# Kernel tuning notes

Measured on AMD Instinct MI355X. Metric: run time of the kernel, lower is better.

## Reference

```python
import jax, jax.numpy as jnp
import numpy as np

B, GRID, IN_CO, OUT_CO = 32, 4096, 64, 64
T_EMB, N_MODES = 256, 512
M_HALF = N_MODES // 2 + 1  # 257 retained rFFT modes


def setup_inputs() -> dict:
    key = jax.random.key(0)
    ks = jax.random.split(key, 6)
    w_std = jnp.sqrt(1.0 / (2.0 * IN_CO))
    return {
        "x": jax.random.normal(ks[0], (B, GRID, IN_CO), jnp.float32),
        "t_emb": jax.random.normal(ks[1], (B, T_EMB), jnp.float32),
        "weights_real": jax.random.normal(ks[2], (M_HALF, IN_CO, OUT_CO), jnp.float32) * w_std,
        "weights_imag": jax.random.normal(ks[3], (M_HALF, IN_CO, OUT_CO), jnp.float32) * w_std,
        "dense_real": jax.random.normal(ks[4], (T_EMB, M_HALF), jnp.float32) * jnp.sqrt(1.0 / T_EMB),
        "dense_imag": jax.random.normal(ks[5], (T_EMB, M_HALF), jnp.float32) * jnp.sqrt(1.0 / T_EMB),
    }


def reference(x, t_emb, weights_real, weights_imag, dense_real, dense_imag):
    b, in_grid_sz, _ = x.shape
    m = weights_real.shape[0]  # n_modes//2 + 1
    weights = weights_real + 1j * weights_imag  # (m, in_co, out_co)
    # rFFT over the grid axis
    x_ft = jnp.fft.rfft(x, axis=-2, norm="forward")  # (b, grid//2+1, in_co) complex
    # time modulation per mode: Dense(real) + i*Dense(imag)
    t_tr = (t_emb @ dense_real) + 1j * (t_emb @ dense_imag)  # (b, m)
    # original einsum with eye == elementwise per-mode scale then per-mode matmul
    x_out = jnp.einsum("bmi,mio->bmo", x_ft[:, :m, :], weights) * t_tr[:, :, None]
    out_ft = jnp.zeros((b, in_grid_sz // 2 + 1, weights.shape[-1]), jnp.complex64)
    out_ft = out_ft.at[:, :m, :].set(x_out)
    return jnp.fft.irfft(out_ft, axis=-2, n=in_grid_sz, norm="forward")
```

## Files before the change

kernel.cpp:

```cpp
#include <hip/hip_runtime.h>
#include <hip/hip_bf16.h>

typedef short short8 __attribute__((ext_vector_type(8)));
typedef float f32x4 __attribute__((ext_vector_type(4)));
typedef const void __attribute__((address_space(1))) as1_void;
typedef void __attribute__((address_space(3))) as3_void;

__device__ __forceinline__ float sin_rev(float r) {
  float o; asm("v_sin_f32 %0, %1" : "=v"(o) : "v"(r)); return o;
}
__device__ __forceinline__ float cos_rev(float r) {
  float o; asm("v_cos_f32 %0, %1" : "=v"(o) : "v"(r)); return o;
}

#define INV4096 0.000244140625f
#define INV16   0.0625f

__global__ __launch_bounds__(256) void prep_kernel(const float* __restrict__ t_emb,
                                                   const float* __restrict__ dr,
                                                   const float* __restrict__ di,
                                                   float* __restrict__ Sr,
                                                   float* __restrict__ Si,
                                                   const float* __restrict__ x,
                                                   __hip_bfloat16* __restrict__ E,
                                                   __hip_bfloat16* __restrict__ O,
                                                   float* __restrict__ Xr256p,
                                                   float* __restrict__ x2048f) {
  const int bid = blockIdx.x;
  const int tid = threadIdx.x;
  __shared__ float te[256];
  __shared__ float tileA[64][65];
  __shared__ float tileB[64][65];
  __shared__ float red[4][64];
  __shared__ float xm[64];

  if (bid < 32) {
    int b = bid;
    te[tid] = t_emb[b * 256 + tid];
    __syncthreads();
    for (int m = tid; m < 257; m += 256) {
      float ar = 0.f, ai = 0.f;
      for (int t = 0; t < 256; ++t) {
        float e = te[t];
        ar += e * dr[t * 257 + m];
        ai += e * di[t * 257 + m];
      }
      float c = (m == 0 ? 1.0f : 2.0f) * (1.0f / 4096.0f);
      Sr[b * 257 + m] = ar * c;
      Si[b * 257 + m] = ai * c;
    }
  } else {
    int idx = bid - 32;
    int nt = idx & 31;
    int b  = idx >> 5;
    int n0 = nt * 64;
    int m0r = (63 - nt) * 64;
#pragma unroll
    for (int it = 0; it < 4; ++it) {
      int c = it * 256 + tid;
      int r = c >> 4, i4 = (c & 15) * 4;
      float4 v = *(const float4*)&x[((size_t)b * 4096 + n0 + r) * 64 + i4];
      tileA[r][i4 + 0] = v.x; tileA[r][i4 + 1] = v.y;
      tileA[r][i4 + 2] = v.z; tileA[r][i4 + 3] = v.w;
      float4 w = *(const float4*)&x[((size_t)b * 4096 + m0r + r) * 64 + i4];
      tileB[r][i4 + 0] = w.x; tileB[r][i4 + 1] = w.y;
      tileB[r][i4 + 2] = w.z; tileB[r][i4 + 3] = w.w;
    }
    if (tid < 64) xm[tid] = (nt > 0) ? x[((size_t)b * 4096 + (4096 - n0)) * 64 + tid] : 0.f;
    __syncthreads();
#pragma unroll
    for (int it = 0; it < 2; ++it) {
      int c  = it * 256 + tid;
      int i  = c >> 3;
      int ch = c & 7;
      union { short8 v; unsigned short u[8]; } pe, po;
#pragma unroll
      for (int jj = 0; jj < 8; ++jj) {
        int j = ch * 8 + jj;
        float a = tileA[j][i];
        float mir = (j == 0) ? xm[i] : tileB[64 - j][i];
        __hip_bfloat16 he = __float2bfloat16(a + mir);
        __hip_bfloat16 ho = __float2bfloat16(a - mir);
        pe.u[jj] = *(unsigned short*)&he;
        po.u[jj] = *(unsigned short*)&ho;
      }
      size_t base = ((size_t)b * 64 + i) * 2048 + n0 + ch * 8;
      *(short8*)&E[base] = pe.v;
      *(short8*)&O[base] = po.v;
    }
    {
      int i = tid & 63, g = tid >> 6;
      float acc = 0.f;
#pragma unroll
      for (int j = 0; j < 16; ++j) {
        float w = cos_rev((float)j * INV16);
        acc += w * (tileA[g * 16 + j][i] + tileB[g * 16 + j][i]);
      }
      red[g][i] = acc;
    }
    __syncthreads();
    if (tid < 64) {
      Xr256p[((size_t)b * 32 + nt) * 64 + tid] =
          red[0][tid] + red[1][tid] + red[2][tid] + red[3][tid];
      if (nt == 31) x2048f[b * 64 + tid] = tileB[0][tid];
    }
  }
}

template <int NF, int MODE>
__device__ __forceinline__ void stage_genT(int m0, int kt,
                                           const __hip_bfloat16* __restrict__ B, int ldb, int n0,
                                           __hip_bfloat16* As, __hip_bfloat16* Bs, int tid) {
#pragma unroll
  for (int j = 0; j < NF; ++j) {
    int c   = j * 256 + tid;
    int row = c >> 3;
    int chg = (c & 7) ^ (row & 7);
    const __hip_bfloat16* gb = B + (size_t)(n0 + row) * ldb + kt + chg * 8;
    __hip_bfloat16* lb = Bs + (size_t)(j * 256 + (tid & 192)) * 8;
    __builtin_amdgcn_global_load_lds((as1_void*)gb, (as3_void*)lb, 16, 0, 0);
  }
#pragma unroll
  for (int j = 0; j < 4; ++j) {
    int c   = j * 256 + tid;
    int row = c >> 3;
    int chg = (c & 7) ^ (row & 7);
    int gr  = m0 + row;
    union { short8 v; unsigned short u[8]; } pk;
#pragma unroll
    for (int jj = 0; jj < 8; ++jj) {
      int col = kt + chg * 8 + jj;
      float v;
      if (MODE == 1) {
        int m  = (gr < 256) ? gr : (gr - 255);
        int ph = (m * col) & 4095;
        v = (gr < 256) ?  cos_rev((float)ph * INV4096)
                       : -sin_rev((float)ph * INV4096);
      } else {
        int k  = (col < 256) ? col : (col - 255);
        int ph = (gr * k) & 4095;
        v = (col < 256) ? cos_rev((float)ph * INV4096)
                        : sin_rev((float)ph * INV4096);
      }
      __hip_bfloat16 h = __float2bfloat16(v);
      pk.u[jj] = *(unsigned short*)&h;
    }
    *(short8*)&As[(size_t)c * 8] = pk.v;
  }
}

template <int NF>
__device__ __forceinline__ void compute_stepT(const __hip_bfloat16* As, const __hip_bfloat16* Bs,
                                              int wr, int wc, int fr, int fq,
                                              f32x4 acc[4][NF]) {
#pragma unroll
  for (int kk = 0; kk < 2; ++kk) {
    short8 av[4], bv[NF];
#pragma unroll
    for (int m = 0; m < 4; ++m) {
      int row  = wr + m * 16 + fr;
      int slot = (fq + kk * 4) ^ (row & 7);
      av[m] = *(const short8*)(As + row * 64 + slot * 8);
    }
#pragma unroll
    for (int n = 0; n < NF; ++n) {
      int row  = wc + n * 16 + fr;
      int slot = (fq + kk * 4) ^ (row & 7);
      bv[n] = *(const short8*)(Bs + row * 64 + slot * 8);
    }
#pragma unroll
    for (int m = 0; m < 4; ++m)
#pragma unroll
      for (int n = 0; n < NF; ++n)
        acc[m][n] = __builtin_amdgcn_mfma_f32_16x16x32_bf16(av[m], bv[n], acc[m][n], 0, 0, 0);
  }
}

template <int NF, int MODE>
__device__ __forceinline__ void gemm_coreT(int m0,
                                           const __hip_bfloat16* __restrict__ B, int ldb, int n0,
                                           int k0, int ksteps,
                                           __hip_bfloat16* As, __hip_bfloat16* Bs,
                                           f32x4 acc[4][NF]) {
  const int tid  = threadIdx.x;
  const int lane = tid & 63;
  const int wv   = tid >> 6;
  const int wr   = (wv >> 1) * 64;
  const int wc   = (wv & 1) * (NF * 16);
  const int fr   = lane & 15;
  const int fq   = lane >> 4;

  for (int ks = 0; ks < ksteps; ++ks) {
    stage_genT<NF, MODE>(m0, k0 + ks * 64, B, ldb, n0, As, Bs, tid);
    __syncthreads();
    compute_stepT<NF>(As, Bs, wr, wc, fr, fq, acc);
    __syncthreads();
  }
}

__global__ __launch_bounds__(256) void gemm1_kernel(const __hip_bfloat16* __restrict__ E,
                                                    const __hip_bfloat16* __restrict__ O,
                                                    __hip_bfloat16* __restrict__ C1,
                                                    int kchunk, int splitk) {
  __shared__ __hip_bfloat16 As[128 * 64];
  __shared__ __hip_bfloat16 Bs[128 * 64];
  int n0 = blockIdx.x * 128;
  int m0 = blockIdx.y * 128;
  int k0 = blockIdx.z * kchunk;
  const __hip_bfloat16* B = (m0 < 256) ? E : O;
  f32x4 acc[4][4];
#pragma unroll
  for (int m = 0; m < 4; ++m)
#pragma unroll
    for (int n = 0; n < 4; ++n)
#pragma unroll
      for (int r = 0; r < 4; ++r) acc[m][n][r] = 0.f;

  gemm_coreT<4, 1>(m0, B, 2048, n0, k0, kchunk >> 6, As, Bs, acc);

  const int lane = threadIdx.x & 63;
  const int wv   = threadIdx.x >> 6;
  const int wr   = (wv >> 1) * 64, wc = (wv & 1) * 64;
  const int fr   = lane & 15, fq = lane >> 4;
#pragma unroll
  for (int m = 0; m < 4; ++m)
#pragma unroll
    for (int n = 0; n < 4; ++n)
#pragma unroll
      for (int j = 0; j < 4; ++j) {
        int row = m0 + wr + m * 16 + fq * 4 + j;
        int col = n0 + wc + n * 16 + fr;
        C1[((size_t)row * splitk + blockIdx.z) * 2048 + col] = __float2bfloat16(acc[m][n][j]);
      }
}

__global__ __launch_bounds__(256) void mix_kernel(const __hip_bfloat16* __restrict__ C1,
                                                  const float* __restrict__ Xr256p,
                                                  const float* __restrict__ x2048f,
                                                  const float* __restrict__ Wr,
                                                  const float* __restrict__ Wi,
                                                  const float* __restrict__ Sr,
                                                  const float* __restrict__ Si,
                                                  __hip_bfloat16* __restrict__ Y2T,
                                                  __hip_bfloat16* __restrict__ Yx,
                                                  int splitk) {
  const int k = blockIdx.x;
  const int q = blockIdx.y;
  const int tid = threadIdx.x;
  __shared__ float wlr[4096];
  __shared__ float wli[4096];
  __shared__ float xs[2048];

  const float* wrg = Wr + (size_t)k * 4096;
  const float* wig = Wi + (size_t)k * 4096;
  for (int c = tid; c < 1024; c += 256) {
    *(float4*)&wlr[c * 4] = *(const float4*)&wrg[c * 4];
    *(float4*)&wli[c * 4] = *(const float4*)&wig[c * 4];
  }

  {
    const int part = tid >> 7;
    const int ln   = tid & 127;
    const int bi0  = q * 1024 + ln * 8;
    float f[8] = {0.f, 0.f, 0.f, 0.f, 0.f, 0.f, 0.f, 0.f};
    if (part == 0) {
      if (k < 256) {
        const __hip_bfloat16* src = C1 + (size_t)k * splitk * 2048 + bi0;
        for (int z = 0; z < splitk; ++z) {
          short8 v = *(const short8*)(src + (size_t)z * 2048);
#pragma unroll
          for (int j = 0; j < 8; ++j) {
            unsigned short u = (unsigned short)v[j];
            f[j] += __bfloat162float(*(__hip_bfloat16*)&u);
          }
        }
        float par = (k & 1) ? -1.f : 1.f;
#pragma unroll
        for (int j = 0; j < 8; ++j) f[j] += par * x2048f[bi0 + j];
      } else {
        const float* sp = Xr256p + (size_t)(bi0 >> 6) * 2048 + (bi0 & 63);
#pragma unroll 8
        for (int nt = 0; nt < 32; ++nt)
#pragma unroll
          for (int j = 0; j < 8; ++j) f[j] += sp[nt * 64 + j];
      }
    } else if (k > 0) {
      const __hip_bfloat16* src = C1 + (size_t)(255 + k) * splitk * 2048 + bi0;
      for (int z = 0; z < splitk; ++z) {
        short8 v = *(const short8*)(src + (size_t)z * 2048);
#pragma unroll
        for (int j = 0; j < 8; ++j) {
          unsigned short u = (unsigned short)v[j];
          f[j] += __bfloat162float(*(__hip_bfloat16*)&u);
        }
      }
    }
#pragma unroll
    for (int j = 0; j < 8; ++j) xs[part * 1024 + ln * 8 + j] = f[j];
  }
  __syncthreads();

  const int o  = tid & 63;
  const int jj = tid >> 6;
  float pr[4] = {0.f, 0.f, 0.f, 0.f};
  float pi[4] = {0.f, 0.f, 0.f, 0.f};
#pragma unroll 4
  for (int i = 0; i < 64; ++i) {
    float wrv = wlr[i * 64 + o];
    float wiv = wli[i * 64 + o];
#pragma unroll
    for (int u = 0; u < 4; ++u) {
      int lb = (jj * 4 + u) * 64 + i;
      float xr = xs[lb], xi = xs[1024 + lb];
      pr[u] += xr * wrv - xi * wiv;
      pi[u] += xr * wiv + xi * wrv;
    }
  }
#pragma unroll
  for (int u = 0; u < 4; ++u) {
    int b = q * 16 + jj * 4 + u;
    float sr = Sr[b * 257 + k], si = Si[b * 257 + k];
    int bo = b * 64 + o;
    __hip_bfloat16 yr = __float2bfloat16(pr[u] * sr - pi[u] * si);
    __hip_bfloat16 yi = __float2bfloat16(pr[u] * si + pi[u] * sr);
    if (k < 256) Y2T[(size_t)bo * 512 + k] = yr;
    else         Yx[bo] = yr;
    if (k >= 1)  Y2T[(size_t)bo * 512 + 255 + k] = yi;
  }
}

__global__ __launch_bounds__(256) void gemm2_kernel(const __hip_bfloat16* __restrict__ Y2T,
                                                    const __hip_bfloat16* __restrict__ Yx,
                                                    float* __restrict__ out) {
  __shared__ __hip_bfloat16 As[128 * 64];
  __shared__ __hip_bfloat16 Bs[64 * 64];
  __shared__ float red2[4][64];
  int n0 = blockIdx.x * 64;
  int m0 = blockIdx.y * 128;
  f32x4 accC[4][2], accS[4][2];
#pragma unroll
  for (int m = 0; m < 4; ++m)
#pragma unroll
    for (int n = 0; n < 2; ++n)
#pragma unroll
      for (int r = 0; r < 4; ++r) { accC[m][n][r] = 0.f; accS[m][n][r] = 0.f; }

  gemm_coreT<2, 2>(m0, Y2T, 512, n0, 0,   4, As, Bs, accC);
  gemm_coreT<2, 2>(m0, Y2T, 512, n0, 256, 4, As, Bs, accS);

  const int lane = threadIdx.x & 63;
  const int wv   = threadIdx.x >> 6;
  const int wr   = (wv >> 1) * 64, wc = (wv & 1) * 32;
  const int fr   = lane & 15, fq = lane >> 4;
  float yx[2];
#pragma unroll
  for (int n = 0; n < 2; ++n)
    yx[n] = __bfloat162float(Yx[n0 + wc + n * 16 + fr]);
#pragma unroll
  for (int m = 0; m < 4; ++m)
#pragma unroll
    for (int j = 0; j < 4; ++j) {
      int row = m0 + wr + m * 16 + fq * 4 + j;
      float g = cos_rev((float)(row & 15) * INV16);
#pragma unroll
      for (int n = 0; n < 2; ++n) {
        int col = n0 + wc + n * 16 + fr;
        int b = col >> 6, o = col & 63;
        float vC = accC[m][n][j] + g * yx[n];
        float vS = accS[m][n][j];
        out[((size_t)b * 4096 + row) * 64 + o] = vC - vS;
        if (row > 0)
          out[((size_t)b * 4096 + (4096 - row)) * 64 + o] = vC + vS;
      }
    }

  if (m0 == 0) {
    __syncthreads();
    const int tid = threadIdx.x;
    int col = tid & 63, grp = tid >> 6;
    int bo = n0 + col;
    float s = 0.f;
    for (int k = grp * 64; k < grp * 64 + 64; ++k) {
      float v = __bfloat162float(Y2T[(size_t)bo * 512 + k]);
      s += (k & 1) ? -v : v;
    }
    red2[grp][col] = s;
    __syncthreads();
    if (tid < 64) {
      int bo2 = n0 + tid;
      float alt = red2[0][tid] + red2[1][tid] + red2[2][tid] + red2[3][tid]
                + __bfloat162float(Yx[bo2]);
      int b = bo2 >> 6, o = bo2 & 63;
      out[((size_t)b * 4096 + 2048) * 64 + o] = alt;
    }
  }
}

extern "C" void kernel_launch(void* const* d_in, const int* in_sizes, int n_in,
                              void* d_out, int out_size, void* d_ws, size_t ws_size,
                              hipStream_t stream) {
  const float* x  = (const float*)d_in[0];
  const float* te = (const float*)d_in[1];
  const float* wr = (const float*)d_in[2];
  const float* wi = (const float*)d_in[3];
  const float* dr = (const float*)d_in[4];
  const float* di = (const float*)d_in[5];
  float* out = (float*)d_out;

  char* p = (char*)d_ws;
  auto alloc = [&](size_t bytes) -> char* {
    char* r = p;
    p += (bytes + 255) & ~(size_t)255;
    return r;
  };
  __hip_bfloat16* E   = (__hip_bfloat16*)alloc(2048ull * 2048 * 2);
  __hip_bfloat16* O   = (__hip_bfloat16*)alloc(2048ull * 2048 * 2);
  float* Xr256p = (float*)alloc(32ull * 32 * 64 * 4);
  float* x2048f = (float*)alloc(2048 * 4);
  float* Sr = (float*)alloc(32 * 257 * 4);
  float* Si = (float*)alloc(32 * 257 * 4);
  __hip_bfloat16* Y2T = (__hip_bfloat16*)alloc(2048ull * 512 * 2);
  __hip_bfloat16* Yx  = (__hip_bfloat16*)alloc(2048 * 2);
  size_t fixed = (size_t)(p - (char*)d_ws);

  int splitk = 2;
  if (ws_size >= fixed + 8ull * 512 * 2048 * 2)      splitk = 8;
  else if (ws_size >= fixed + 4ull * 512 * 2048 * 2) splitk = 4;
  __hip_bfloat16* C1 = (__hip_bfloat16*)alloc((size_t)splitk * 512 * 2048 * 2);
  int kchunk = 2048 / splitk;

  prep_kernel<<<1056, 256, 0, stream>>>(te, dr, di, Sr, Si, x, E, O, Xr256p, x2048f);
  gemm1_kernel<<<dim3(16, 4, splitk), 256, 0, stream>>>(E, O, C1, kchunk, splitk);
  mix_kernel<<<dim3(257, 2), 256, 0, stream>>>(C1, Xr256p, x2048f, wr, wi, Sr, Si, Y2T, Yx, splitk);
  gemm2_kernel<<<dim3(32, 16), 256, 0, stream>>>(Y2T, Yx, out);
}
```

Baseline: 85.54 us.

## Fuse four stages into one persistent cooperative kernel with grid syncs

Converts the prep, gemm1, mix and gemm2 kernels into device task functions. They run inside a single persistent cooperative kernel, with grid-wide barriers between stages and a shared LDS buffer. The goal is to remove the launch gaps and tail drain between four separate kernel launches. In exchange, occupancy is capped at two blocks per CU, grid.sync adds its own overhead, and per-stage parallelism is limited to at most 512 resident blocks. Split-K is now fixed at 8, and a separate-kernel fallback remains in place.

```diff
diff --git a/kernel.cpp b/kernel.cpp
--- a/kernel.cpp
+++ b/kernel.cpp
@@ -1,5 +1,8 @@
 #include <hip/hip_runtime.h>
 #include <hip/hip_bf16.h>
+#include <hip/hip_cooperative_groups.h>
+
+namespace cg = cooperative_groups;
 
 typedef short short8 __attribute__((ext_vector_type(8)));
 typedef float f32x4 __attribute__((ext_vector_type(4)));
@@ -15,24 +18,26 @@
 
 #define INV4096 0.000244140625f
 #define INV16   0.0625f
-
-__global__ __launch_bounds__(256) void prep_kernel(const float* __restrict__ t_emb,
-                                                   const float* __restrict__ dr,
-                                                   const float* __restrict__ di,
-                                                   float* __restrict__ Sr,
-                                                   float* __restrict__ Si,
-                                                   const float* __restrict__ x,
-                                                   __hip_bfloat16* __restrict__ E,
-                                                   __hip_bfloat16* __restrict__ O,
-                                                   float* __restrict__ Xr256p,
-                                                   float* __restrict__ x2048f) {
-  const int bid = blockIdx.x;
-  const int tid = threadIdx.x;
-  __shared__ float te[256];
-  __shared__ float tileA[64][65];
-  __shared__ float tileB[64][65];
-  __shared__ float red[4][64];
-  __shared__ float xm[64];
+#define SPLITK  8
+#define KCHUNK  256
+
+__device__ __forceinline__ void prep_task(int bid, int tid, char* smem,
+                                          const float* __restrict__ t_emb,
+                                          const float* __restrict__ dr,
+                                          const float* __restrict__ di,
+                                          float* __restrict__ Sr,
+                                          float* __restrict__ Si,
+                                          const float* __restrict__ x,
+                                          __hip_bfloat16* __restrict__ E,
+                                          __hip_bfloat16* __restrict__ O,
+                                          float* __restrict__ Xr256p,
+                                          float* __restrict__ x2048f) {
+  float* sf    = (float*)smem;
+  float* tileA = sf;
+  float* tileB = sf + 4160;
+  float* te    = sf + 8320;
+  float* red   = sf + 8576;
+  float* xm    = sf + 8832;
 
   if (bid < 32) {
     int b = bid;
@@ -60,11 +65,11 @@
       int c = it * 256 + tid;
       int r = c >> 4, i4 = (c & 15) * 4;
       float4 v = *(const float4*)&x[((size_t)b * 4096 + n0 + r) * 64 + i4];
-      tileA[r][i4 + 0] = v.x; tileA[r][i4 + 1] = v.y;
-      tileA[r][i4 + 2] = v.z; tileA[r][i4 + 3] = v.w;
+      tileA[r * 65 + i4 + 0] = v.x; tileA[r * 65 + i4 + 1] = v.y;
+      tileA[r * 65 + i4 + 2] = v.z; tileA[r * 65 + i4 + 3] = v.w;
       float4 w = *(const float4*)&x[((size_t)b * 4096 + m0r + r) * 64 + i4];
-      tileB[r][i4 + 0] = w.x; tileB[r][i4 + 1] = w.y;
-      tileB[r][i4 + 2] = w.z; tileB[r][i4 + 3] = w.w;
+      tileB[r * 65 + i4 + 0] = w.x; tileB[r * 65 + i4 + 1] = w.y;
+      tileB[r * 65 + i4 + 2] = w.z; tileB[r * 65 + i4 + 3] = w.w;
     }
     if (tid < 64) xm[tid] = (nt > 0) ? x[((size_t)b * 4096 + (4096 - n0)) * 64 + tid] : 0.f;
     __syncthreads();
@@ -77,8 +82,8 @@
 #pragma unroll
       for (int jj = 0; jj < 8; ++jj) {
         int j = ch * 8 + jj;
-        float a = tileA[j][i];
-        float mir = (j == 0) ? xm[i] : tileB[64 - j][i];
+        float a = tileA[j * 65 + i];
+        float mir = (j == 0) ? xm[i] : tileB[(64 - j) * 65 + i];
         __hip_bfloat16 he = __float2bfloat16(a + mir);
         __hip_bfloat16 ho = __float2bfloat16(a - mir);
         pe.u[jj] = *(unsigned short*)&he;
@@ -94,15 +99,15 @@
 #pragma unroll
       for (int j = 0; j < 16; ++j) {
         float w = cos_rev((float)j * INV16);
-        acc += w * (tileA[g * 16 + j][i] + tileB[g * 16 + j][i]);
-      }
-      red[g][i] = acc;
+        acc += w * (tileA[(g * 16 + j) * 65 + i] + tileB[(g * 16 + j) * 65 + i]);
+      }
+      red[g * 64 + i] = acc;
     }
     __syncthreads();
     if (tid < 64) {
       Xr256p[((size_t)b * 32 + nt) * 64 + tid] =
-          red[0][tid] + red[1][tid] + red[2][tid] + red[3][tid];
-      if (nt == 31) x2048f[b * 64 + tid] = tileB[0][tid];
+          red[tid] + red[64 + tid] + red[128 + tid] + red[192 + tid];
+      if (nt == 31) x2048f[b * 64 + tid] = tileB[0 * 65 + tid];
     }
   }
 }
@@ -198,15 +203,17 @@
   }
 }
 
-__global__ __launch_bounds__(256) void gemm1_kernel(const __hip_bfloat16* __restrict__ E,
-                                                    const __hip_bfloat16* __restrict__ O,
-                                                    __hip_bfloat16* __restrict__ C1,
-                                                    int kchunk, int splitk) {
-  __shared__ __hip_bfloat16 As[128 * 64];
-  __shared__ __hip_bfloat16 Bs[128 * 64];
-  int n0 = blockIdx.x * 128;
-  int m0 = blockIdx.y * 128;
-  int k0 = blockIdx.z * kchunk;
+__device__ __forceinline__ void gemm1_task(int t, char* smem,
+                                           const __hip_bfloat16* __restrict__ E,
+                                           const __hip_bfloat16* __restrict__ O,
+                                           __hip_bfloat16* __restrict__ C1) {
+  __hip_bfloat16* As = (__hip_bfloat16*)smem;
+  __hip_bfloat16* Bs = (__hip_bfloat16*)smem + 8192;
+  int z   = t >> 6;
+  int rem = t & 63;
+  int m0  = (rem >> 4) * 128;
+  int n0  = (rem & 15) * 128;
+  int k0  = z * KCHUNK;
   const __hip_bfloat16* B = (m0 < 256) ? E : O;
   f32x4 acc[4][4];
 #pragma unroll
@@ -216,7 +223,7 @@
 #pragma unroll
       for (int r = 0; r < 4; ++r) acc[m][n][r] = 0.f;
 
-  gemm_coreT<4, 1>(m0, B, 2048, n0, k0, kchunk >> 6, As, Bs, acc);
+  gemm_coreT<4, 1>(m0, B, 2048, n0, k0, KCHUNK >> 6, As, Bs, acc);
 
   const int lane = threadIdx.x & 63;
   const int wv   = threadIdx.x >> 6;
@@ -230,26 +237,25 @@
       for (int j = 0; j < 4; ++j) {
         int row = m0 + wr + m * 16 + fq * 4 + j;
         int col = n0 + wc + n * 16 + fr;
-        C1[((size_t)row * splitk + blockIdx.z) * 2048 + col] = __float2bfloat16(acc[m][n][j]);
-      }
-}
-
-__global__ __launch_bounds__(256) void mix_kernel(const __hip_bfloat16* __restrict__ C1,
-                                                  const float* __restrict__ Xr256p,
-                                                  const float* __restrict__ x2048f,
-                                                  const float* __restrict__ Wr,
-                                                  const float* __restrict__ Wi,
-                                                  const float* __restrict__ Sr,
-                                                  const float* __restrict__ Si,
-                                                  __hip_bfloat16* __restrict__ Y2T,
-                                                  __hip_bfloat16* __restrict__ Yx,
-                                                  int splitk) {
-  const int k = blockIdx.x;
-  const int q = blockIdx.y;
-  const int tid = threadIdx.x;
-  __shared__ float wlr[4096];
-  __shared__ float wli[4096];
-  __shared__ float xs[2048];
+        C1[((size_t)row * SPLITK + z) * 2048 + col] = __float2bfloat16(acc[m][n][j]);
+      }
+}
+
+__device__ __forceinline__ void mix_task(int t, int tid, char* smem,
+                                         const __hip_bfloat16* __restrict__ C1,
+                                         const float* __restrict__ Xr256p,
+                                         const float* __restrict__ x2048f,
+                                         const float* __restrict__ Wr,
+                                         const float* __restrict__ Wi,
+                                         const float* __restrict__ Sr,
+                                         const float* __restrict__ Si,
+                                         __hip_bfloat16* __restrict__ Y2T,
+                                         __hip_bfloat16* __restrict__ Yx) {
+  float* wlr = (float*)smem;
+  float* wli = wlr + 4096;
+  float* xs  = wli + 4096;
+  const int k = t % 257;
+  const int q = t / 257;
 
   const float* wrg = Wr + (size_t)k * 4096;
   const float* wig = Wi + (size_t)k * 4096;
@@ -265,8 +271,8 @@
     float f[8] = {0.f, 0.f, 0.f, 0.f, 0.f, 0.f, 0.f, 0.f};
     if (part == 0) {
       if (k < 256) {
-        const __hip_bfloat16* src = C1 + (size_t)k * splitk * 2048 + bi0;
-        for (int z = 0; z < splitk; ++z) {
+        const __hip_bfloat16* src = C1 + (size_t)k * SPLITK * 2048 + bi0;
+        for (int z = 0; z < SPLITK; ++z) {
           short8 v = *(const short8*)(src + (size_t)z * 2048);
 #pragma unroll
           for (int j = 0; j < 8; ++j) {
@@ -285,8 +291,8 @@
           for (int j = 0; j < 8; ++j) f[j] += sp[nt * 64 + j];
       }
     } else if (k > 0) {
-      const __hip_bfloat16* src = C1 + (size_t)(255 + k) * splitk * 2048 + bi0;
-      for (int z = 0; z < splitk; ++z) {
+      const __hip_bfloat16* src = C1 + (size_t)(255 + k) * SPLITK * 2048 + bi0;
+      for (int z = 0; z < SPLITK; ++z) {
         short8 v = *(const short8*)(src + (size_t)z * 2048);
 #pragma unroll
         for (int j = 0; j < 8; ++j) {
@@ -329,14 +335,15 @@
   }
 }
 
-__global__ __launch_bounds__(256) void gemm2_kernel(const __hip_bfloat16* __restrict__ Y2T,
-                                                    const __hip_bfloat16* __restrict__ Yx,
-                                                    float* __restrict__ out) {
-  __shared__ __hip_bfloat16 As[128 * 64];
-  __shared__ __hip_bfloat16 Bs[64 * 64];
-  __shared__ float red2[4][64];
-  int n0 = blockIdx.x * 64;
-  int m0 = blockIdx.y * 128;
+__device__ __forceinline__ void gemm2_task(int t, char* smem,
+                                           const __hip_bfloat16* __restrict__ Y2T,
+                                           const __hip_bfloat16* __restrict__ Yx,
+                                           float* __restrict__ out) {
+  __hip_bfloat16* As = (__hip_bfloat16*)smem;
+  __hip_bfloat16* Bs = (__hip_bfloat16*)smem + 8192;
+  float* red2 = (float*)(smem + 24576);
+  int n0 = (t & 31) * 64;
+  int m0 = (t >> 5) * 128;
   f32x4 accC[4][2], accS[4][2];
 #pragma unroll
   for (int m = 0; m < 4; ++m)
@@ -384,16 +391,86 @@
       float v = __bfloat162float(Y2T[(size_t)bo * 512 + k]);
       s += (k & 1) ? -v : v;
     }
-    red2[grp][col] = s;
+    red2[grp * 64 + col] = s;
     __syncthreads();
     if (tid < 64) {
       int bo2 = n0 + tid;
-      float alt = red2[0][tid] + red2[1][tid] + red2[2][tid] + red2[3][tid]
+      float alt = red2[tid] + red2[64 + tid] + red2[128 + tid] + red2[192 + tid]
                 + __bfloat162float(Yx[bo2]);
       int b = bo2 >> 6, o = bo2 & 63;
       out[((size_t)b * 4096 + 2048) * 64 + o] = alt;
     }
   }
+}
+
+__global__ __launch_bounds__(256, 2) void mega_kernel(const float* __restrict__ t_emb,
+                                                      const float* __restrict__ dr,
+                                                      const float* __restrict__ di,
+                                                      float* __restrict__ Sr,
+                                                      float* __restrict__ Si,
+                                                      const float* __restrict__ x,
+                                                      __hip_bfloat16* __restrict__ E,
+                                                      __hip_bfloat16* __restrict__ O,
+                                                      float* __restrict__ Xr256p,
+                                                      float* __restrict__ x2048f,
+                                                      const float* __restrict__ Wr,
+                                                      const float* __restrict__ Wi,
+                                                      __hip_bfloat16* __restrict__ C1,
+                                                      __hip_bfloat16* __restrict__ Y2T,
+                                                      __hip_bfloat16* __restrict__ Yx,
+                                                      float* __restrict__ out) {
+  __shared__ __align__(16) char smem[40960];
+  const int tid = threadIdx.x;
+  cg::grid_group grid = cg::this_grid();
+
+  for (int t = blockIdx.x; t < 1056; t += gridDim.x) {
+    prep_task(t, tid, smem, t_emb, dr, di, Sr, Si, x, E, O, Xr256p, x2048f);
+    __syncthreads();
+  }
+  grid.sync();
+  for (int t = blockIdx.x; t < 512; t += gridDim.x) {
+    gemm1_task(t, smem, E, O, C1);
+    __syncthreads();
+  }
+  grid.sync();
+  for (int t = blockIdx.x; t < 514; t += gridDim.x) {
+    mix_task(t, tid, smem, C1, Xr256p, x2048f, Wr, Wi, Sr, Si, Y2T, Yx);
+    __syncthreads();
+  }
+  grid.sync();
+  for (int t = blockIdx.x; t < 512; t += gridDim.x) {
+    gemm2_task(t, smem, Y2T, Yx, out);
+    __syncthreads();
+  }
+}
+
+__global__ __launch_bounds__(256) void prep_sep(const float* t_emb, const float* dr,
+                                                const float* di, float* Sr, float* Si,
+                                                const float* x, __hip_bfloat16* E,
+                                                __hip_bfloat16* O, float* Xr256p,
+                                                float* x2048f) {
+  __shared__ __align__(16) char smem[35840];
+  prep_task(blockIdx.x, threadIdx.x, smem, t_emb, dr, di, Sr, Si, x, E, O, Xr256p, x2048f);
+}
+__global__ __launch_bounds__(256) void gemm1_sep(const __hip_bfloat16* E,
+                                                 const __hip_bfloat16* O,
+                                                 __hip_bfloat16* C1) {
+  __shared__ __align__(16) char smem[32768];
+  gemm1_task(blockIdx.x, smem, E, O, C1);
+}
+__global__ __launch_bounds__(256) void mix_sep(const __hip_bfloat16* C1, const float* Xr256p,
+                                               const float* x2048f, const float* Wr,
+                                               const float* Wi, const float* Sr,
+                                               const float* Si, __hip_bfloat16* Y2T,
+                                               __hip_bfloat16* Yx) {
+  __shared__ __align__(16) char smem[40960];
+  mix_task(blockIdx.x, threadIdx.x, smem, C1, Xr256p, x2048f, Wr, Wi, Sr, Si, Y2T, Yx);
+}
+__global__ __launch_bounds__(256) void gemm2_sep(const __hip_bfloat16* Y2T,
+                                                 const __hip_bfloat16* Yx,
+                                                 float* out) {
+  __shared__ __align__(16) char smem[25600];
+  gemm2_task(blockIdx.x, smem, Y2T, Yx, out);
 }
 
 extern "C" void kernel_launch(void* const* d_in, const int* in_sizes, int n_in,
@@ -421,16 +498,39 @@
   float* Si = (float*)alloc(32 * 257 * 4);
   __hip_bfloat16* Y2T = (__hip_bfloat16*)alloc(2048ull * 512 * 2);
   __hip_bfloat16* Yx  = (__hip_bfloat16*)alloc(2048 * 2);
-  size_t fixed = (size_t)(p - (char*)d_ws);
-
-  int splitk = 2;
-  if (ws_size >= fixed + 8ull * 512 * 2048 * 2)      splitk = 8;
-  else if (ws_size >= fixed + 4ull * 512 * 2048 * 2) splitk = 4;
-  __hip_bfloat16* C1 = (__hip_bfloat16*)alloc((size_t)splitk * 512 * 2048 * 2);
-  int kchunk = 2048 / splitk;
-
-  prep_kernel<<<1056, 256, 0, stream>>>(te, dr, di, Sr, Si, x, E, O, Xr256p, x2048f);
-  gemm1_kernel<<<dim3(16, 4, splitk), 256, 0, stream>>>(E, O, C1, kchunk, splitk);
-  mix_kernel<<<dim3(257, 2), 256, 0, stream>>>(C1, Xr256p, x2048f, wr, wi, Sr, Si, Y2T, Yx, splitk);
-  gemm2_kernel<<<dim3(32, 16), 256, 0, stream>>>(Y2T, Yx, out);
-}
+  __hip_bfloat16* C1  = (__hip_bfloat16*)alloc((size_t)SPLITK * 512 * 2048 * 2);
+
+  bool coop = false;
+  int grid = 0;
+  {
+    int dev = 0;
+    (void)hipGetDevice(&dev);
+    int supported = 0;
+    if (hipDeviceGetAttribute(&supported, hipDeviceAttributeCooperativeLaunch, dev) == hipSuccess
+        && supported) {
+      int occ = 0;
+      if (hipOccupancyMaxActiveBlocksPerMultiprocessor(&occ, (const void*)mega_kernel, 256, 0)
+              == hipSuccess && occ >= 1) {
+        grid = occ * 256;
+        if (grid > 512) grid = 512;
+        coop = true;
+      }
+    }
+  }
+
+  if (coop) {
+    void* args[] = {
+      (void*)&te, (void*)&dr, (void*)&di, (void*)&Sr, (void*)&Si,
+      (void*)&x,  (void*)&E,  (void*)&O,  (void*)&Xr256p, (void*)&x2048f,
+      (void*)&wr, (void*)&wi, (void*)&C1, (void*)&Y2T, (void*)&Yx, (void*)&out
+    };
+    hipError_t le = hipLaunchCooperativeKernel((void*)mega_kernel, dim3(grid), dim3(256),
+                                               args, 0, stream);
+    if (le == hipSuccess) return;
+  }
+
+  prep_sep<<<1056, 256, 0, stream>>>(te, dr, di, Sr, Si, x, E, O, Xr256p, x2048f);
+  gemm1_sep<<<512, 256, 0, stream>>>(E, O, C1);
+  mix_sep<<<514, 256, 0, stream>>>(C1, Xr256p, x2048f, wr, wi, Sr, Si, Y2T, Yx);
+  gemm2_sep<<<512, 256, 0, stream>>>(Y2T, Yx, out);
+}
```

New measurement: 298.1 us. +248.5%, slower.
